# Performance work log

Hardware: AMD Instinct MI355X
Metric: run time of the kernel (lower is better)

Reference implementation:

```python
import jax, jax.numpy as jnp
import numpy as np
from jax import lax

INPUT_DIM = 64
HIDDEN = 128
NUM_CLASSES = 3


def _uniform(key, shape, scale):
    return jax.random.uniform(key, shape, jnp.float32, -scale, scale)


def setup_inputs() -> dict:
    key = jax.random.key(0)
    ks = jax.random.split(key, 16)
    s = 1.0 / np.sqrt(HIDDEN)
    inp = {
        "x": jax.random.normal(ks[0], (256, 512, INPUT_DIM), jnp.float32),
        # layer 0 LSTM params (PyTorch gate order: i, f, g, o)
        "W_ih0": _uniform(ks[1], (4 * HIDDEN, INPUT_DIM), s),
        "W_hh0": _uniform(ks[2], (4 * HIDDEN, HIDDEN), s),
        "b_ih0": _uniform(ks[3], (4 * HIDDEN,), s),
        "b_hh0": _uniform(ks[4], (4 * HIDDEN,), s),
        # layer 1 LSTM params
        "W_ih1": _uniform(ks[5], (4 * HIDDEN, HIDDEN), s),
        "W_hh1": _uniform(ks[6], (4 * HIDDEN, HIDDEN), s),
        "b_ih1": _uniform(ks[7], (4 * HIDDEN,), s),
        "b_hh1": _uniform(ks[8], (4 * HIDDEN,), s),
        # MLP head: fc1 (H -> H//2), fc2 (H//2 -> num_classes)
        "W1": _uniform(ks[9], (HIDDEN // 2, HIDDEN), s),
        "b1": _uniform(ks[10], (HIDDEN // 2,), s),
        "W2": _uniform(ks[11], (NUM_CLASSES, HIDDEN // 2), 1.0 / np.sqrt(HIDDEN // 2)),
        "b2": _uniform(ks[12], (NUM_CLASSES,), 1.0 / np.sqrt(HIDDEN // 2)),
    }
    return inp


def _lstm_layer(x, W_ih, W_hh, b_ih, b_hh):
    # x: [B, T, I] -> ys: [B, T, H]
    B = x.shape[0]
    H = W_hh.shape[1]
    b = b_ih + b_hh

    def step(carry, xt):
        h, c = carry
        g = xt @ W_ih.T + h @ W_hh.T + b  # [B, 4H]
        i, f, gg, o = jnp.split(g, 4, axis=-1)
        c = jax.nn.sigmoid(f) * c + jax.nn.sigmoid(i) * jnp.tanh(gg)
        h = jax.nn.sigmoid(o) * jnp.tanh(c)
        return (h, c), h

    h0 = jnp.zeros((B, H), x.dtype)
    (_, _), ys = lax.scan(step, (h0, h0), jnp.swapaxes(x, 0, 1))
    return jnp.swapaxes(ys, 0, 1)


def reference(x, W_ih0, W_hh0, b_ih0, b_hh0, W_ih1, W_hh1, b_ih1, b_hh1, W1, b1, W2, b2):
    # Eval mode: dropout layers are identity.
    h = _lstm_layer(x, W_ih0, W_hh0, b_ih0, b_hh0)   # [B, T, H]
    h = _lstm_layer(h, W_ih1, W_hh1, b_ih1, b_hh1)   # [B, T, H]
    last = h[:, -1, :]                                # [B, H]
    out = jax.nn.relu(last @ W1.T + b1) @ W2.T + b2   # [B, num_classes]
    return out
```

## Files before the change

kernel.cpp:

```cpp
#include <hip/hip_runtime.h>
#include <hip/hip_bf16.h>
#include <stdint.h>

#define BATCH 256
#define SEQ   512
#define INDIM 64
#define H     128
#define RB    4
#define NTILE (BATCH / RB)
#define CH    16
#define NCH   (SEQ / CH)

using short8  = __attribute__((ext_vector_type(8))) short;
using float4v = __attribute__((ext_vector_type(4))) float;

#define LOG2E 1.4426950408889634f

__device__ __forceinline__ unsigned short f2bf(float f) {
    union { float f; uint32_t u; } v; v.f = f;
    uint32_t u = v.u;
    return (unsigned short)((u + 0x7FFFu + ((u >> 16) & 1u)) >> 16);
}

__device__ __forceinline__ float fast_exp2(float x) {
#if __has_builtin(__builtin_amdgcn_exp2f)
    return __builtin_amdgcn_exp2f(x);
#else
    return __expf(x * 0.6931471805599453f);
#endif
}
__device__ __forceinline__ float fast_rcp(float x) {
#if __has_builtin(__builtin_amdgcn_rcpf)
    return __builtin_amdgcn_rcpf(x);
#else
    return 1.f / x;
#endif
}
__device__ __forceinline__ float sigmoid_fast(float x) {
    return fast_rcp(1.f + fast_exp2(-LOG2E * x));
}
__device__ __forceinline__ float tanh_fast(float x) {
    return fmaf(-2.f, fast_rcp(1.f + fast_exp2((2.f * LOG2E) * x)), 1.f);
}

__device__ __forceinline__ void light_barrier() {
    asm volatile("s_waitcnt lgkmcnt(0)\n\ts_barrier" ::: "memory");
}

__global__ void conv_x_kernel(const float* __restrict__ x,
                              unsigned short* __restrict__ xb, int n4,
                              int* __restrict__ flags) {
    int i = blockIdx.x * blockDim.x + threadIdx.x;
    if (blockIdx.x == 0 && threadIdx.x < NTILE) flags[threadIdx.x] = 0;
    if (i >= n4) return;
    float4 f = ((const float4*)x)[i];
    ushort4 o;
    o.x = f2bf(f.x); o.y = f2bf(f.y); o.z = f2bf(f.z); o.w = f2bf(f.w);
    ((ushort4*)xb)[i] = o;
}

template<int KIN, bool IS_PROD>
__device__ __forceinline__ void lstm_body(
    const unsigned short* __restrict__ xin,
    const float* __restrict__ Wih,
    const float* __restrict__ Whh,
    const float* __restrict__ b_ih, const float* __restrict__ b_hh,
    unsigned short* __restrict__ outseq,
    const float* __restrict__ W1, const float* __restrict__ b1,
    const float* __restrict__ W2, const float* __restrict__ b2,
    float* __restrict__ out,
    int* flag, int bt)
{
    constexpr int KT  = KIN / 32;
    constexpr int PAD = 132;
    const int lane = threadIdx.x & 63;
    const int quad = lane >> 4;
    const int l16  = lane & 15;
    const int b0   = bt * RB;
    const int cell = (threadIdx.x >> 6) * 16 + l16;
    const int arow = l16 & 12;
    const int xrow = b0 + (l16 >> 2);

    __shared__ short hbuf[2][16][PAD];
    __shared__ float hl[RB][128];
    __shared__ float mid[RB][65];
    for (int i = threadIdx.x; i < 2 * 16 * PAD; i += 512) ((short*)hbuf)[i] = 0;

    short8 whh_f[4][4];
    short8 wih_f[4][KT];
    float  bias[4];
#pragma unroll
    for (int tT = 0; tT < 4; tT++) {
        const int n = tT * 128 + cell;
#pragma unroll
        for (int kt = 0; kt < 4; kt++) {
            const float* p = Whh + (size_t)n * H + kt * 32 + quad * 8;
            float4 f0 = *(const float4*)p;
            float4 f1 = *(const float4*)(p + 4);
            short8 s;
            s[0]=f2bf(f0.x); s[1]=f2bf(f0.y); s[2]=f2bf(f0.z); s[3]=f2bf(f0.w);
            s[4]=f2bf(f1.x); s[5]=f2bf(f1.y); s[6]=f2bf(f1.z); s[7]=f2bf(f1.w);
            whh_f[tT][kt] = s;
        }
#pragma unroll
        for (int kt = 0; kt < KT; kt++) {
            const float* p = Wih + (size_t)n * KIN + kt * 32 + quad * 8;
            float4 f0 = *(const float4*)p;
            float4 f1 = *(const float4*)(p + 4);
            short8 s;
            s[0]=f2bf(f0.x); s[1]=f2bf(f0.y); s[2]=f2bf(f0.z); s[3]=f2bf(f0.w);
            s[4]=f2bf(f1.x); s[5]=f2bf(f1.y); s[6]=f2bf(f1.z); s[7]=f2bf(f1.w);
            wih_f[tT][kt] = s;
        }
        bias[tT] = b_ih[n] + b_hh[n];
    }

    float c0 = 0.f;

    const unsigned short* xp = xin + ((size_t)xrow * SEQ) * KIN + quad * 8;
    unsigned short* op = nullptr;
    if (IS_PROD)
        op = outseq + ((size_t)(b0 + quad) * SEQ) * H + cell;

    short8  xf0[KT], xf1[KT];
    float4v accA[4], accB[4];
    __syncthreads();

    auto halfstep = [&](int t, int CUR,
                        float4v (&accUse)[4], float4v (&accNext)[4],
                        short8 (&xPre)[KT], short8 (&xNext)[KT],
                        bool doPre, bool doNext) __attribute__((always_inline)) {
        short8 ha[4];
#pragma unroll
        for (int kt = 0; kt < 4; kt++)
            ha[kt] = *(const short8*)&hbuf[CUR][arow][kt * 32 + quad * 8];
#pragma unroll
        for (int tT = 0; tT < 4; tT++)
#pragma unroll
            for (int kt = 0; kt < 4; kt++)
                accUse[tT] = __builtin_amdgcn_mfma_f32_16x16x32_bf16(ha[kt], whh_f[tT][kt], accUse[tT], 0, 0, 0);
        float g0 = accUse[0][0], g1 = accUse[1][0], g2 = accUse[2][0], g3 = accUse[3][0];

        if (doPre) {
            const unsigned short* p = xp + (size_t)(t + 2) * KIN;
#pragma unroll
            for (int kt = 0; kt < KT; kt++) xPre[kt] = *(const short8*)(p + kt * 32);
        }
        if (doNext) {
#pragma unroll
            for (int tT = 0; tT < 4; tT++)
                accNext[tT] = (float4v){bias[tT], bias[tT], bias[tT], bias[tT]};
#pragma unroll
            for (int tT = 0; tT < 4; tT++)
#pragma unroll
                for (int kt = 0; kt < KT; kt++)
                    accNext[tT] = __builtin_amdgcn_mfma_f32_16x16x32_bf16(xNext[kt], wih_f[tT][kt], accNext[tT], 0, 0, 0);
        }

        float si = sigmoid_fast(g0);
        float sf = sigmoid_fast(g1);
        float tg = tanh_fast(g2);
        float so = sigmoid_fast(g3);
        float cn = fmaf(sf, c0, si * tg);
        c0 = cn;
        float h = so * tanh_fast(cn);
        const unsigned short hb = f2bf(h);
        hbuf[CUR ^ 1][quad * 4][cell] = (short)hb;
        if (IS_PROD) {
            *op = hb;
            op += H;
        } else if (t == SEQ - 1) {
            hl[quad][cell] = h;
        }
        light_barrier();
    };

    for (int ch = 0; ch < NCH; ch++) {
        const int t0 = ch * CH;
        if (!IS_PROD) {
            if (threadIdx.x == 0) {
                while (__hip_atomic_load(flag, __ATOMIC_RELAXED, __HIP_MEMORY_SCOPE_AGENT) <= ch)
                    __builtin_amdgcn_s_sleep(2);
                (void)__hip_atomic_load(flag, __ATOMIC_ACQUIRE, __HIP_MEMORY_SCOPE_AGENT);
            }
            __syncthreads();
        }
        if (!IS_PROD || ch == 0) {
            const unsigned short* p0 = xp + (size_t)t0 * KIN;
            const unsigned short* p1 = p0 + KIN;
#pragma unroll
            for (int kt = 0; kt < KT; kt++) {
                xf0[kt] = *(const short8*)(p0 + kt * 32);
                xf1[kt] = *(const short8*)(p1 + kt * 32);
            }
#pragma unroll
            for (int tT = 0; tT < 4; tT++)
                accA[tT] = (float4v){bias[tT], bias[tT], bias[tT], bias[tT]};
#pragma unroll
            for (int tT = 0; tT < 4; tT++)
#pragma unroll
                for (int kt = 0; kt < KT; kt++)
                    accA[tT] = __builtin_amdgcn_mfma_f32_16x16x32_bf16(xf0[kt], wih_f[tT][kt], accA[tT], 0, 0, 0);
        }

#pragma unroll 1
        for (int i = 0; i < CH; i += 2) {
            const int t = t0 + i;
            const bool preA  = IS_PROD ? (t + 2 < SEQ) : (i + 2 < CH);
            const bool preB  = IS_PROD ? (t + 3 < SEQ) : (i + 3 < CH);
            const bool nextA = IS_PROD ? (t + 2 < SEQ) : (i + 2 < CH);
            halfstep(t,     0, accA, accB, xf0, xf1, preA, true);
            halfstep(t + 1, 1, accB, accA, xf1, xf0, preB, nextA);
        }
        __syncthreads();
        if (IS_PROD && threadIdx.x == 0)
            __hip_atomic_fetch_add(flag, 1, __ATOMIC_RELEASE, __HIP_MEMORY_SCOPE_AGENT);
    }

    if (!IS_PROD) {
        if (threadIdx.x < RB * 64) {
            const int row = threadIdx.x >> 6, j = threadIdx.x & 63;
            float s = b1[j];
            const float* wr = W1 + (size_t)j * 128;
#pragma unroll 8
            for (int k = 0; k < 128; k++) s = fmaf(hl[row][k], wr[k], s);
            mid[row][j] = fmaxf(s, 0.f);
        }
        __syncthreads();
        if (threadIdx.x < RB * 3) {
            const int row = threadIdx.x / 3, k = threadIdx.x - row * 3;
            float o = b2[k];
            const float* wr = W2 + (size_t)k * 64;
#pragma unroll 8
            for (int j = 0; j < 64; j++) o = fmaf(mid[row][j], wr[j], o);
            out[(size_t)(b0 + row) * 3 + k] = o;
        }
    }
}

__global__ __launch_bounds__(512, 2)
void lstm_fused_kernel(const unsigned short* __restrict__ xb,
                       const float* __restrict__ Wih0, const float* __restrict__ Whh0,
                       const float* __restrict__ bih0, const float* __restrict__ bhh0,
                       const float* __restrict__ Wih1, const float* __restrict__ Whh1,
                       const float* __restrict__ bih1, const float* __restrict__ bhh1,
                       unsigned short* __restrict__ h0sq,
                       const float* __restrict__ W1, const float* __restrict__ b1,
                       const float* __restrict__ W2, const float* __restrict__ b2,
                       float* __restrict__ out,
                       int* __restrict__ flags)
{
    const int bt = blockIdx.x & (NTILE - 1);
    if (blockIdx.x < NTILE)
        lstm_body<64,  true >(xb,   Wih0, Whh0, bih0, bhh0, h0sq,
                              W1, b1, W2, b2, out, flags + bt, bt);
    else
        lstm_body<128, false>(h0sq, Wih1, Whh1, bih1, bhh1, nullptr,
                              W1, b1, W2, b2, out, flags + bt, bt);
}

extern "C" void kernel_launch(void* const* d_in, const int* in_sizes, int n_in,
                              void* d_out, int out_size, void* d_ws, size_t ws_size,
                              hipStream_t stream) {
    const float* x     = (const float*)d_in[0];
    const float* W_ih0 = (const float*)d_in[1];
    const float* W_hh0 = (const float*)d_in[2];
    const float* b_ih0 = (const float*)d_in[3];
    const float* b_hh0 = (const float*)d_in[4];
    const float* W_ih1 = (const float*)d_in[5];
    const float* W_hh1 = (const float*)d_in[6];
    const float* b_ih1 = (const float*)d_in[7];
    const float* b_hh1 = (const float*)d_in[8];
    const float* W1    = (const float*)d_in[9];
    const float* b1    = (const float*)d_in[10];
    const float* W2    = (const float*)d_in[11];
    const float* b2    = (const float*)d_in[12];
    float* out = (float*)d_out;

    char* ws = (char*)d_ws;
    unsigned short* xb    = (unsigned short*)ws;
    unsigned short* h0sq  = (unsigned short*)(ws + 16777216);
    int*            flags = (int*)(ws + 50331648);

    conv_x_kernel<<<8192, 256, 0, stream>>>(x, xb, (BATCH * SEQ * INDIM) / 4, flags);
    lstm_fused_kernel<<<2 * NTILE, 512, 0, stream>>>(xb, W_ih0, W_hh0, b_ih0, b_hh0,
                                                     W_ih1, W_hh1, b_ih1, b_hh1,
                                                     h0sq, W1, b1, W2, b2, out, flags);
}
```

Before: 509.1 us.

## Process two batch tiles per block to interleave independent LSTM recurrences

Each workgroup now advances two independent 4-row batch tiles in lockstep, interleaving their MFMA chains and gate math. The goal is to hide MFMA and transcendental latency on the serial recurrence and to share each barrier across two tiles, with half as many workgroups. The input projection is no longer pipelined one step ahead; it is computed inline right before the recurrent MFMAs within each step. The costs are fewer blocks (64 instead of 128), more registers per thread, and a longer per-step critical path.

```diff
diff --git a/kernel.cpp b/kernel.cpp
--- a/kernel.cpp
+++ b/kernel.cpp
@@ -8,6 +8,7 @@
 #define H     128
 #define RB    4
 #define NTILE (BATCH / RB)
+#define NPAIR (NTILE / 2)
 #define CH    16
 #define NCH   (SEQ / CH)
 
@@ -51,7 +52,7 @@
                               unsigned short* __restrict__ xb, int n4,
                               int* __restrict__ flags) {
     int i = blockIdx.x * blockDim.x + threadIdx.x;
-    if (blockIdx.x == 0 && threadIdx.x < NTILE) flags[threadIdx.x] = 0;
+    if (blockIdx.x == 0 && threadIdx.x < NPAIR) flags[threadIdx.x] = 0;
     if (i >= n4) return;
     float4 f = ((const float4*)x)[i];
     ushort4 o;
@@ -69,22 +70,26 @@
     const float* __restrict__ W1, const float* __restrict__ b1,
     const float* __restrict__ W2, const float* __restrict__ b2,
     float* __restrict__ out,
-    int* flag, int bt)
+    int* flag, int pt)
 {
     constexpr int KT  = KIN / 32;
     constexpr int PAD = 132;
     const int lane = threadIdx.x & 63;
     const int quad = lane >> 4;
     const int l16  = lane & 15;
-    const int b0   = bt * RB;
+    const int b0A  = (2 * pt) * RB;
+    const int b0B  = (2 * pt + 1) * RB;
     const int cell = (threadIdx.x >> 6) * 16 + l16;
     const int arow = l16 & 12;
-    const int xrow = b0 + (l16 >> 2);
-
-    __shared__ short hbuf[2][16][PAD];
-    __shared__ float hl[RB][128];
-    __shared__ float mid[RB][65];
-    for (int i = threadIdx.x; i < 2 * 16 * PAD; i += 512) ((short*)hbuf)[i] = 0;
+
+    __shared__ short hbA[2][16][PAD];
+    __shared__ short hbB[2][16][PAD];
+    __shared__ float hl[2][RB][128];
+    __shared__ float mid[2][RB][65];
+    for (int i = threadIdx.x; i < 2 * 16 * PAD; i += 512) {
+        ((short*)hbA)[i] = 0;
+        ((short*)hbB)[i] = 0;
+    }
 
     short8 whh_f[4][4];
     short8 wih_f[4][KT];
@@ -115,62 +120,86 @@
         bias[tT] = b_ih[n] + b_hh[n];
     }
 
-    float c0 = 0.f;
-
-    const unsigned short* xp = xin + ((size_t)xrow * SEQ) * KIN + quad * 8;
-    unsigned short* op = nullptr;
-    if (IS_PROD)
-        op = outseq + ((size_t)(b0 + quad) * SEQ) * H + cell;
-
-    short8  xf0[KT], xf1[KT];
+    float c0A = 0.f, c0B = 0.f;
+
+    const unsigned short* xpA = xin + ((size_t)(b0A + (l16 >> 2)) * SEQ) * KIN + quad * 8;
+    const unsigned short* xpB = xin + ((size_t)(b0B + (l16 >> 2)) * SEQ) * KIN + quad * 8;
+    unsigned short* opA = nullptr;
+    unsigned short* opB = nullptr;
+    if (IS_PROD) {
+        opA = outseq + ((size_t)(b0A + quad) * SEQ) * H + cell;
+        opB = outseq + ((size_t)(b0B + quad) * SEQ) * H + cell;
+    }
+
+    short8  xfA[KT], xfB[KT];
     float4v accA[4], accB[4];
+#pragma unroll
+    for (int tT = 0; tT < 4; tT++) {
+        accA[tT] = (float4v){bias[tT], bias[tT], bias[tT], bias[tT]};
+        accB[tT] = (float4v){bias[tT], bias[tT], bias[tT], bias[tT]};
+    }
     __syncthreads();
 
-    auto halfstep = [&](int t, int CUR,
-                        float4v (&accUse)[4], float4v (&accNext)[4],
-                        short8 (&xPre)[KT], short8 (&xNext)[KT],
-                        bool doPre, bool doNext) __attribute__((always_inline)) {
-        short8 ha[4];
-#pragma unroll
-        for (int kt = 0; kt < 4; kt++)
-            ha[kt] = *(const short8*)&hbuf[CUR][arow][kt * 32 + quad * 8];
+    auto dualstep = [&](int t, int CUR, bool doPre) __attribute__((always_inline)) {
+        short8 haA[4], haB[4];
+#pragma unroll
+        for (int kt = 0; kt < 4; kt++) {
+            haA[kt] = *(const short8*)&hbA[CUR][arow][kt * 32 + quad * 8];
+            haB[kt] = *(const short8*)&hbB[CUR][arow][kt * 32 + quad * 8];
+        }
+#pragma unroll
+        for (int tT = 0; tT < 4; tT++) {
+            accA[tT][0] = bias[tT];
+            accB[tT][0] = bias[tT];
+        }
 #pragma unroll
         for (int tT = 0; tT < 4; tT++)
 #pragma unroll
-            for (int kt = 0; kt < 4; kt++)
-                accUse[tT] = __builtin_amdgcn_mfma_f32_16x16x32_bf16(ha[kt], whh_f[tT][kt], accUse[tT], 0, 0, 0);
-        float g0 = accUse[0][0], g1 = accUse[1][0], g2 = accUse[2][0], g3 = accUse[3][0];
-
+            for (int kt = 0; kt < KT; kt++) {
+                accA[tT] = __builtin_amdgcn_mfma_f32_16x16x32_bf16(xfA[kt], wih_f[tT][kt], accA[tT], 0, 0, 0);
+                accB[tT] = __builtin_amdgcn_mfma_f32_16x16x32_bf16(xfB[kt], wih_f[tT][kt], accB[tT], 0, 0, 0);
+            }
         if (doPre) {
-            const unsigned short* p = xp + (size_t)(t + 2) * KIN;
-#pragma unroll
-            for (int kt = 0; kt < KT; kt++) xPre[kt] = *(const short8*)(p + kt * 32);
-        }
-        if (doNext) {
-#pragma unroll
-            for (int tT = 0; tT < 4; tT++)
-                accNext[tT] = (float4v){bias[tT], bias[tT], bias[tT], bias[tT]};
-#pragma unroll
-            for (int tT = 0; tT < 4; tT++)
-#pragma unroll
-                for (int kt = 0; kt < KT; kt++)
-                    accNext[tT] = __builtin_amdgcn_mfma_f32_16x16x32_bf16(xNext[kt], wih_f[tT][kt], accNext[tT], 0, 0, 0);
-        }
-
-        float si = sigmoid_fast(g0);
-        float sf = sigmoid_fast(g1);
-        float tg = tanh_fast(g2);
-        float so = sigmoid_fast(g3);
-        float cn = fmaf(sf, c0, si * tg);
-        c0 = cn;
-        float h = so * tanh_fast(cn);
-        const unsigned short hb = f2bf(h);
-        hbuf[CUR ^ 1][quad * 4][cell] = (short)hb;
+            const unsigned short* pA = xpA + (size_t)(t + 1) * KIN;
+            const unsigned short* pB = xpB + (size_t)(t + 1) * KIN;
+#pragma unroll
+            for (int kt = 0; kt < KT; kt++) {
+                xfA[kt] = *(const short8*)(pA + kt * 32);
+                xfB[kt] = *(const short8*)(pB + kt * 32);
+            }
+        }
+#pragma unroll
+        for (int tT = 0; tT < 4; tT++)
+#pragma unroll
+            for (int kt = 0; kt < 4; kt++) {
+                accA[tT] = __builtin_amdgcn_mfma_f32_16x16x32_bf16(haA[kt], whh_f[tT][kt], accA[tT], 0, 0, 0);
+                accB[tT] = __builtin_amdgcn_mfma_f32_16x16x32_bf16(haB[kt], whh_f[tT][kt], accB[tT], 0, 0, 0);
+            }
+        float gA0 = accA[0][0], gA1 = accA[1][0], gA2 = accA[2][0], gA3 = accA[3][0];
+        float gB0 = accB[0][0], gB1 = accB[1][0], gB2 = accB[2][0], gB3 = accB[3][0];
+
+        float siA = sigmoid_fast(gA0);
+        float siB = sigmoid_fast(gB0);
+        float sfA = sigmoid_fast(gA1);
+        float sfB = sigmoid_fast(gB1);
+        float tgA = tanh_fast(gA2);
+        float tgB = tanh_fast(gB2);
+        float soA = sigmoid_fast(gA3);
+        float soB = sigmoid_fast(gB3);
+        c0A = fmaf(sfA, c0A, siA * tgA);
+        c0B = fmaf(sfB, c0B, siB * tgB);
+        float hA = soA * tanh_fast(c0A);
+        float hB = soB * tanh_fast(c0B);
+        const unsigned short hbfA = f2bf(hA);
+        const unsigned short hbfB = f2bf(hB);
+        hbA[CUR ^ 1][quad * 4][cell] = (short)hbfA;
+        hbB[CUR ^ 1][quad * 4][cell] = (short)hbfB;
         if (IS_PROD) {
-            *op = hb;
-            op += H;
+            *opA = hbfA; opA += H;
+            *opB = hbfB; opB += H;
         } else if (t == SEQ - 1) {
-            hl[quad][cell] = h;
+            hl[0][quad][cell] = hA;
+            hl[1][quad][cell] = hB;
         }
         light_barrier();
     };
@@ -186,31 +215,22 @@
             __syncthreads();
         }
         if (!IS_PROD || ch == 0) {
-            const unsigned short* p0 = xp + (size_t)t0 * KIN;
-            const unsigned short* p1 = p0 + KIN;
+            const unsigned short* pA = xpA + (size_t)t0 * KIN;
+            const unsigned short* pB = xpB + (size_t)t0 * KIN;
 #pragma unroll
             for (int kt = 0; kt < KT; kt++) {
-                xf0[kt] = *(const short8*)(p0 + kt * 32);
-                xf1[kt] = *(const short8*)(p1 + kt * 32);
-            }
-#pragma unroll
-            for (int tT = 0; tT < 4; tT++)
-                accA[tT] = (float4v){bias[tT], bias[tT], bias[tT], bias[tT]};
-#pragma unroll
-            for (int tT = 0; tT < 4; tT++)
-#pragma unroll
-                for (int kt = 0; kt < KT; kt++)
-                    accA[tT] = __builtin_amdgcn_mfma_f32_16x16x32_bf16(xf0[kt], wih_f[tT][kt], accA[tT], 0, 0, 0);
+                xfA[kt] = *(const short8*)(pA + kt * 32);
+                xfB[kt] = *(const short8*)(pB + kt * 32);
+            }
         }
 
 #pragma unroll 1
         for (int i = 0; i < CH; i += 2) {
             const int t = t0 + i;
-            const bool preA  = IS_PROD ? (t + 2 < SEQ) : (i + 2 < CH);
-            const bool preB  = IS_PROD ? (t + 3 < SEQ) : (i + 3 < CH);
-            const bool nextA = IS_PROD ? (t + 2 < SEQ) : (i + 2 < CH);
-            halfstep(t,     0, accA, accB, xf0, xf1, preA, true);
-            halfstep(t + 1, 1, accB, accA, xf1, xf0, preB, nextA);
+            const bool pre0 = IS_PROD ? (t + 1 < SEQ) : (i + 1 < CH);
+            const bool pre1 = IS_PROD ? (t + 2 < SEQ) : (i + 2 < CH);
+            dualstep(t,     0, pre0);
+            dualstep(t + 1, 1, pre1);
         }
         __syncthreads();
         if (IS_PROD && threadIdx.x == 0)
@@ -218,22 +238,25 @@
     }
 
     if (!IS_PROD) {
-        if (threadIdx.x < RB * 64) {
-            const int row = threadIdx.x >> 6, j = threadIdx.x & 63;
+        const int tl  = threadIdx.x >> 8;
+        const int q   = threadIdx.x & 255;
+        const int b0t = tl ? b0B : b0A;
+        {
+            const int row = q >> 6, j = q & 63;
             float s = b1[j];
             const float* wr = W1 + (size_t)j * 128;
 #pragma unroll 8
-            for (int k = 0; k < 128; k++) s = fmaf(hl[row][k], wr[k], s);
-            mid[row][j] = fmaxf(s, 0.f);
+            for (int k = 0; k < 128; k++) s = fmaf(hl[tl][row][k], wr[k], s);
+            mid[tl][row][j] = fmaxf(s, 0.f);
         }
         __syncthreads();
-        if (threadIdx.x < RB * 3) {
-            const int row = threadIdx.x / 3, k = threadIdx.x - row * 3;
+        if (q < RB * 3) {
+            const int row = q / 3, k = q - row * 3;
             float o = b2[k];
             const float* wr = W2 + (size_t)k * 64;
 #pragma unroll 8
-            for (int j = 0; j < 64; j++) o = fmaf(mid[row][j], wr[j], o);
-            out[(size_t)(b0 + row) * 3 + k] = o;
+            for (int j = 0; j < 64; j++) o = fmaf(mid[tl][row][j], wr[j], o);
+            out[(size_t)(b0t + row) * 3 + k] = o;
         }
     }
 }
@@ -250,13 +273,13 @@
                        float* __restrict__ out,
                        int* __restrict__ flags)
 {
-    const int bt = blockIdx.x & (NTILE - 1);
-    if (blockIdx.x < NTILE)
+    const int pt = blockIdx.x & (NPAIR - 1);
+    if (blockIdx.x < NPAIR)
         lstm_body<64,  true >(xb,   Wih0, Whh0, bih0, bhh0, h0sq,
-                              W1, b1, W2, b2, out, flags + bt, bt);
+                              W1, b1, W2, b2, out, flags + pt, pt);
     else
         lstm_body<128, false>(h0sq, Wih1, Whh1, bih1, bhh1, nullptr,
-                              W1, b1, W2, b2, out, flags + bt, bt);
+                              W1, b1, W2, b2, out, flags + pt, pt);
 }
 
 extern "C" void kernel_launch(void* const* d_in, const int* in_sizes, int n_in,
@@ -283,7 +306,7 @@
     int*            flags = (int*)(ws + 50331648);
 
     conv_x_kernel<<<8192, 256, 0, stream>>>(x, xb, (BATCH * SEQ * INDIM) / 4, flags);
-    lstm_fused_kernel<<<2 * NTILE, 512, 0, stream>>>(xb, W_ih0, W_hh0, b_ih0, b_hh0,
+    lstm_fused_kernel<<<2 * NPAIR, 512, 0, stream>>>(xb, W_ih0, W_hh0, b_ih0, b_hh0,
                                                      W_ih1, W_hh1, b_ih1, b_hh1,
                                                      h0sq, W1, b1, W2, b2, out, flags);
 }
```

Result: slower. 776.5 us (+52.5%).

## Split recurrent MFMA chains into two accumulators and drop x-projection lookahead

Applied to the files above, without the earlier changes.

Restructures the per-step LSTM gate computation. The input projection is no longer precomputed one step ahead. Each step now builds the input and recurrent MFMA products itself, interleaved across two independent accumulators that are summed at the end, which halves the serial dependency chain on the critical path. It also replaces the software bf16 rounding with the hardware v_cvt_pk_bf16_f32 instruction. In exchange, the input-projection MFMAs now run inside each serial step instead of overlapping with the previous step's activations.

```diff
diff --git a/kernel.cpp b/kernel.cpp
--- a/kernel.cpp
+++ b/kernel.cpp
@@ -122,52 +122,70 @@
     if (IS_PROD)
         op = outseq + ((size_t)(b0 + quad) * SEQ) * H + cell;
 
-    short8  xf0[KT], xf1[KT];
-    float4v accA[4], accB[4];
+    short8 xf0[KT], xf1[KT];
     __syncthreads();
 
-    auto halfstep = [&](int t, int CUR,
-                        float4v (&accUse)[4], float4v (&accNext)[4],
-                        short8 (&xPre)[KT], short8 (&xNext)[KT],
-                        bool doPre, bool doNext) __attribute__((always_inline)) {
+    auto step = [&](int t, int CUR, short8 (&xf)[KT],
+                    bool doPre) __attribute__((always_inline)) {
         short8 ha[4];
 #pragma unroll
         for (int kt = 0; kt < 4; kt++)
             ha[kt] = *(const short8*)&hbuf[CUR][arow][kt * 32 + quad * 8];
-#pragma unroll
-        for (int tT = 0; tT < 4; tT++)
-#pragma unroll
-            for (int kt = 0; kt < 4; kt++)
-                accUse[tT] = __builtin_amdgcn_mfma_f32_16x16x32_bf16(ha[kt], whh_f[tT][kt], accUse[tT], 0, 0, 0);
-        float g0 = accUse[0][0], g1 = accUse[1][0], g2 = accUse[2][0], g3 = accUse[3][0];
-
+
+        float4v accA[4], accB[4];
+#pragma unroll
+        for (int tT = 0; tT < 4; tT++) {
+            accA[tT] = (float4v){bias[tT], bias[tT], bias[tT], bias[tT]};
+            accB[tT] = (float4v){0.f, 0.f, 0.f, 0.f};
+        }
+#pragma unroll
+        for (int tT = 0; tT < 4; tT++)
+            accA[tT] = __builtin_amdgcn_mfma_f32_16x16x32_bf16(xf[0], wih_f[tT][0], accA[tT], 0, 0, 0);
+#pragma unroll
+        for (int tT = 0; tT < 4; tT++)
+            accA[tT] = __builtin_amdgcn_mfma_f32_16x16x32_bf16(xf[1], wih_f[tT][1], accA[tT], 0, 0, 0);
+        if constexpr (KT == 4) {
+#pragma unroll
+            for (int tT = 0; tT < 4; tT++)
+                accB[tT] = __builtin_amdgcn_mfma_f32_16x16x32_bf16(xf[2], wih_f[tT][2], accB[tT], 0, 0, 0);
+#pragma unroll
+            for (int tT = 0; tT < 4; tT++)
+                accB[tT] = __builtin_amdgcn_mfma_f32_16x16x32_bf16(xf[3], wih_f[tT][3], accB[tT], 0, 0, 0);
+        }
         if (doPre) {
             const unsigned short* p = xp + (size_t)(t + 2) * KIN;
 #pragma unroll
-            for (int kt = 0; kt < KT; kt++) xPre[kt] = *(const short8*)(p + kt * 32);
-        }
-        if (doNext) {
-#pragma unroll
-            for (int tT = 0; tT < 4; tT++)
-                accNext[tT] = (float4v){bias[tT], bias[tT], bias[tT], bias[tT]};
-#pragma unroll
-            for (int tT = 0; tT < 4; tT++)
-#pragma unroll
-                for (int kt = 0; kt < KT; kt++)
-                    accNext[tT] = __builtin_amdgcn_mfma_f32_16x16x32_bf16(xNext[kt], wih_f[tT][kt], accNext[tT], 0, 0, 0);
-        }
+            for (int kt = 0; kt < KT; kt++) xf[kt] = *(const short8*)(p + kt * 32);
+        }
+#pragma unroll
+        for (int tT = 0; tT < 4; tT++)
+            accA[tT] = __builtin_amdgcn_mfma_f32_16x16x32_bf16(ha[0], whh_f[tT][0], accA[tT], 0, 0, 0);
+#pragma unroll
+        for (int tT = 0; tT < 4; tT++)
+            accB[tT] = __builtin_amdgcn_mfma_f32_16x16x32_bf16(ha[2], whh_f[tT][2], accB[tT], 0, 0, 0);
+#pragma unroll
+        for (int tT = 0; tT < 4; tT++)
+            accA[tT] = __builtin_amdgcn_mfma_f32_16x16x32_bf16(ha[1], whh_f[tT][1], accA[tT], 0, 0, 0);
+#pragma unroll
+        for (int tT = 0; tT < 4; tT++)
+            accB[tT] = __builtin_amdgcn_mfma_f32_16x16x32_bf16(ha[3], whh_f[tT][3], accB[tT], 0, 0, 0);
+
+        float g0 = accA[0][0] + accB[0][0];
+        float g1 = accA[1][0] + accB[1][0];
+        float g2 = accA[2][0] + accB[2][0];
+        float g3 = accA[3][0] + accB[3][0];
 
         float si = sigmoid_fast(g0);
         float sf = sigmoid_fast(g1);
         float tg = tanh_fast(g2);
         float so = sigmoid_fast(g3);
-        float cn = fmaf(sf, c0, si * tg);
-        c0 = cn;
-        float h = so * tanh_fast(cn);
-        const unsigned short hb = f2bf(h);
-        hbuf[CUR ^ 1][quad * 4][cell] = (short)hb;
+        c0 = fmaf(sf, c0, si * tg);
+        float h = so * tanh_fast(c0);
+        uint32_t hp;
+        asm("v_cvt_pk_bf16_f32 %0, %1, %2" : "=v"(hp) : "v"(h), "v"(h));
+        hbuf[CUR ^ 1][quad * 4][cell] = (short)(hp & 0xffffu);
         if (IS_PROD) {
-            *op = hb;
+            *op = (unsigned short)(hp & 0xffffu);
             op += H;
         } else if (t == SEQ - 1) {
             hl[quad][cell] = h;
@@ -193,24 +211,15 @@
                 xf0[kt] = *(const short8*)(p0 + kt * 32);
                 xf1[kt] = *(const short8*)(p1 + kt * 32);
             }
-#pragma unroll
-            for (int tT = 0; tT < 4; tT++)
-                accA[tT] = (float4v){bias[tT], bias[tT], bias[tT], bias[tT]};
-#pragma unroll
-            for (int tT = 0; tT < 4; tT++)
-#pragma unroll
-                for (int kt = 0; kt < KT; kt++)
-                    accA[tT] = __builtin_amdgcn_mfma_f32_16x16x32_bf16(xf0[kt], wih_f[tT][kt], accA[tT], 0, 0, 0);
         }
 
 #pragma unroll 1
         for (int i = 0; i < CH; i += 2) {
             const int t = t0 + i;
-            const bool preA  = IS_PROD ? (t + 2 < SEQ) : (i + 2 < CH);
-            const bool preB  = IS_PROD ? (t + 3 < SEQ) : (i + 3 < CH);
-            const bool nextA = IS_PROD ? (t + 2 < SEQ) : (i + 2 < CH);
-            halfstep(t,     0, accA, accB, xf0, xf1, preA, true);
-            halfstep(t + 1, 1, accB, accA, xf1, xf0, preB, nextA);
+            const bool pre0 = IS_PROD ? (t + 2 < SEQ) : (i + 2 < CH);
+            const bool pre1 = IS_PROD ? (t + 3 < SEQ) : (i + 3 < CH);
+            step(t,     0, xf0, pre0);
+            step(t + 1, 1, xf1, pre1);
         }
         __syncthreads();
         if (IS_PROD && threadIdx.x == 0)
```

Measured after the change: 472.6 us. 7.2% less time.
